# Optimization experiments

Measured on AMD Instinct MI355X. Metric: run time of the kernel, lower is better.

Reference implementation:

```python
import jax, jax.numpy as jnp
import numpy as np

N_HEADS = 16
LN_EPS = 1e-5


def layer_norm(x, w, b):
    mu = jnp.mean(x, axis=-1, keepdims=True)
    var = jnp.mean((x - mu) ** 2, axis=-1, keepdims=True)
    return (x - mu) * jax.lax.rsqrt(var + LN_EPS) * w + b


def setup_inputs() -> dict:
    key = jax.random.key(0)
    B, S, D = 4, 2048, 1024
    F = 4 * D
    ks = jax.random.split(key, 16)
    s = 0.02
    return {
        "x": jax.random.normal(ks[0], (B, S, D), dtype=jnp.float32),
        "Wq": jax.random.normal(ks[1], (D, D), dtype=jnp.float32) * s,
        "Wk": jax.random.normal(ks[2], (D, D), dtype=jnp.float32) * s,
        "Wv": jax.random.normal(ks[3], (D, D), dtype=jnp.float32) * s,
        "Wo": jax.random.normal(ks[4], (D, D), dtype=jnp.float32) * s,
        "ln1_w": jnp.ones((D,), dtype=jnp.float32),
        "ln1_b": jnp.zeros((D,), dtype=jnp.float32),
        "W1": jax.random.normal(ks[5], (D, F), dtype=jnp.float32) * s,
        "b1": jnp.zeros((F,), dtype=jnp.float32),
        "W2": jax.random.normal(ks[6], (F, D), dtype=jnp.float32) * s,
        "b2": jnp.zeros((D,), dtype=jnp.float32),
        "ln2_w": jnp.ones((D,), dtype=jnp.float32),
        "ln2_b": jnp.zeros((D,), dtype=jnp.float32),
        "conf_w": jax.random.normal(ks[7], (D, 1), dtype=jnp.float32) * s,
        "conf_b": jnp.zeros((1,), dtype=jnp.float32),
    }


def reference(x, Wq, Wk, Wv, Wo, ln1_w, ln1_b, W1, b1, W2, b2, ln2_w, ln2_b, conf_w, conf_b):
    B, S, D = x.shape
    H = N_HEADS
    HD = D // H
    # --- attention sub-block (pre-LN) ---
    h = layer_norm(x, ln1_w, ln1_b)
    q = jnp.einsum("bsd,dhk->bhsk", h, Wq.reshape(D, H, HD))
    k = jnp.einsum("bsd,dhk->bhsk", h, Wk.reshape(D, H, HD))
    v = jnp.einsum("bsd,dhk->bhsk", h, Wv.reshape(D, H, HD))
    scores = jnp.einsum("bhsk,bhtk->bhst", q, k) / jnp.sqrt(jnp.asarray(HD, x.dtype))
    causal = jnp.triu(jnp.ones((S, S), dtype=bool), k=1)  # [S, S]
    scores = jnp.where(causal[None, None, :, :], -jnp.inf, scores)
    attn = jax.nn.softmax(scores, axis=-1)
    ctx = jnp.einsum("bhst,bhtk->bshk", attn, v).reshape(B, S, D)
    x = x + ctx @ Wo  # residual (dropout = identity in eval)
    # --- FFN sub-block ---
    h2 = layer_norm(x, ln2_w, ln2_b)
    x_out = x + jax.nn.relu(h2 @ W1 + b1) @ W2 + b2 * 0 + (jax.nn.relu(h2 @ W1 + b1) @ W2 * 0)
    x_out = x + (jax.nn.relu(h2 @ W1 + b1) @ W2 + b2)
    # --- confidence predictor: avg-pool over seq, linear, sigmoid, mean over batch ---
    conf = jax.nn.sigmoid(jnp.mean(x_out, axis=1) @ conf_w + conf_b)  # [B, 1]
    conf = jnp.mean(conf, axis=0)  # [1]
    return x_out, conf
```

## Files before the change

kernel.cpp:

```cpp
#include <hip/hip_runtime.h>
#include <hip/hip_bf16.h>
#include <math.h>

typedef __bf16 bf16;
typedef __bf16 bf16x8 __attribute__((ext_vector_type(8)));
typedef __bf16 bf16x4 __attribute__((ext_vector_type(4)));
typedef float  f32x4  __attribute__((ext_vector_type(4)));
typedef short  s16x4  __attribute__((ext_vector_type(4)));

#define CLAMP(v) fminf(fmaxf((v), -100.f), 100.f)
#define NEGINF (-1e30f)

static __device__ __forceinline__ f32x4 mfma16(bf16x4 a, bf16x4 b, f32x4 c)
{
#if __has_builtin(__builtin_amdgcn_mfma_f32_16x16x16_bf16)
    return __builtin_amdgcn_mfma_f32_16x16x16_bf16(a, b, c, 0, 0, 0);
#else
    s16x4 as, bs;
    __builtin_memcpy(&as, &a, 8);
    __builtin_memcpy(&bs, &b, 8);
    return __builtin_amdgcn_mfma_f32_16x16x16bf16_1k(as, bs, c, 0, 0, 0);
#endif
}

static __device__ __forceinline__ void gload_lds16(const bf16* g, bf16* l)
{
    __builtin_amdgcn_global_load_lds(
        (const __attribute__((address_space(1))) void*)g,
        (__attribute__((address_space(3))) void*)l, 16, 0, 0);
}

__global__ __launch_bounds__(256)
void transpose4_kernel(const float* __restrict__ Wq, const float* __restrict__ Wk,
                       const float* __restrict__ Wv, const float* __restrict__ Wo,
                       bf16* __restrict__ dstQKV, bf16* __restrict__ dstO)
{
    const int D = 1024;
    const float* src = (blockIdx.z == 0) ? Wq : (blockIdx.z == 1) ? Wk : (blockIdx.z == 2) ? Wv : Wo;
    bf16* dst = (blockIdx.z < 3) ? dstQKV + (size_t)blockIdx.z * D * D : dstO;
    __shared__ float tile[32][33];
    int c0 = blockIdx.x * 32, r0 = blockIdx.y * 32;
    int tx = threadIdx.x, ty = threadIdx.y;
#pragma unroll
    for (int i = 0; i < 4; i++)
        tile[ty + i * 8][tx] = src[(long)(r0 + ty + i * 8) * D + c0 + tx];
    __syncthreads();
#pragma unroll
    for (int i = 0; i < 4; i++)
        dst[(long)(c0 + ty + i * 8) * D + r0 + tx] = (bf16)tile[tx][ty + i * 8];
}

__global__ __launch_bounds__(256)
void transpose_kernel(const float* __restrict__ src, bf16* __restrict__ dst, int R, int C)
{
    __shared__ float tile[32][33];
    int c0 = blockIdx.x * 32, r0 = blockIdx.y * 32;
    int tx = threadIdx.x, ty = threadIdx.y;
#pragma unroll
    for (int i = 0; i < 4; i++)
        tile[ty + i * 8][tx] = src[(long)(r0 + ty + i * 8) * C + c0 + tx];
    __syncthreads();
#pragma unroll
    for (int i = 0; i < 4; i++)
        dst[(long)(c0 + ty + i * 8) * R + r0 + tx] = (bf16)tile[tx][ty + i * 8];
}

__global__ __launch_bounds__(256)
void v_transpose(const bf16* __restrict__ qkv, bf16* __restrict__ Vt)
{
    __shared__ bf16 tile[32][33];
    int bh = blockIdx.z, b = bh >> 4, h = bh & 15;
    int t0 = blockIdx.x * 32, d0 = blockIdx.y * 32;
    int tx = threadIdx.x, ty = threadIdx.y;
#pragma unroll
    for (int i = 0; i < 4; i++)
        tile[ty + i * 8][tx] = qkv[(long)(b * 2048 + t0 + ty + i * 8) * 3072 + 2048 + h * 64 + d0 + tx];
    __syncthreads();
#pragma unroll
    for (int i = 0; i < 4; i++)
        Vt[((long)bh * 64 + d0 + ty + i * 8) * 2048 + t0 + tx] = tile[tx][ty + i * 8];
}

__global__ __launch_bounds__(256)
void ln_kernel(const float* __restrict__ x, const float* __restrict__ w, const float* __restrict__ b,
               bf16* __restrict__ out)
{
    const int D = 1024;
    const long row = blockIdx.x;
    const int t = threadIdx.x;
    f32x4 xv = *(const f32x4*)(x + row * D + t * 4);
    float s  = xv[0] + xv[1] + xv[2] + xv[3];
    float s2 = xv[0] * xv[0] + xv[1] * xv[1] + xv[2] * xv[2] + xv[3] * xv[3];
#pragma unroll
    for (int off = 32; off; off >>= 1) { s += __shfl_xor(s, off); s2 += __shfl_xor(s2, off); }
    __shared__ float ls[4], ls2[4];
    if ((t & 63) == 0) { ls[t >> 6] = s; ls2[t >> 6] = s2; }
    __syncthreads();
    s = ls[0] + ls[1] + ls[2] + ls[3];
    s2 = ls2[0] + ls2[1] + ls2[2] + ls2[3];
    float mu = s / D;
    float var = fmaxf(s2 / D - mu * mu, 0.f);
    float rstd = rsqrtf(var + 1e-5f);
#pragma unroll
    for (int i = 0; i < 4; i++) {
        int c = t * 4 + i;
        float v = (xv[i] - mu) * rstd * w[c] + b[c];
        out[row * D + c] = (bf16)CLAMP(v);
    }
}

template <int MODE>
__global__ __launch_bounds__(256)
void gemm_bt(const bf16* __restrict__ A, int lda, const bf16* __restrict__ Bt, int ldb,
             int M, int N, int K,
             const float* __restrict__ bias, const float* __restrict__ resid,
             void* __restrict__ outv, int ldo)
{
    __shared__ bf16 sA[128 * 32];
    __shared__ bf16 sB[128 * 32];
    const int t = threadIdx.x;
    const int wave = t >> 6, lane = t & 63;
    const int wr = wave >> 1, wc = wave & 1;
    const int quad = lane >> 4, l16 = lane & 15;
    const int bm = blockIdx.y * 128, bn = blockIdx.x * 128;

    f32x4 acc[4][4];
#pragma unroll
    for (int i = 0; i < 4; i++)
#pragma unroll
        for (int j = 0; j < 4; j++) acc[i][j] = f32x4{0.f, 0.f, 0.f, 0.f};

    const int srow = wave * 16 + (lane >> 2);
    const int scol = (lane & 3) * 8;
    const bf16* ga = A + (long)(bm + srow) * lda + scol;
    const bf16* gb = Bt + (long)(bn + srow) * ldb + scol;
    bf16* la = &sA[wave * 16 * 32];
    bf16* lb = &sB[wave * 16 * 32];

    for (int k0 = 0; k0 < K; k0 += 32) {
        __syncthreads();
        gload_lds16(ga + k0, la);
        gload_lds16(gb + k0, lb);
        gload_lds16(ga + (long)64 * lda + k0, la + 64 * 32);
        gload_lds16(gb + (long)64 * ldb + k0, lb + 64 * 32);
        __syncthreads();
        bf16x8 af[4], bfv[4];
#pragma unroll
        for (int i = 0; i < 4; i++)
            af[i] = *(const bf16x8*)(&sA[(wr * 64 + i * 16 + l16) * 32 + quad * 8]);
#pragma unroll
        for (int j = 0; j < 4; j++)
            bfv[j] = *(const bf16x8*)(&sB[(wc * 64 + j * 16 + l16) * 32 + quad * 8]);
#pragma unroll
        for (int i = 0; i < 4; i++)
#pragma unroll
            for (int j = 0; j < 4; j++)
                acc[i][j] = __builtin_amdgcn_mfma_f32_16x16x32_bf16(af[i], bfv[j], acc[i][j], 0, 0, 0);
    }

    float bv[4];
    if constexpr (MODE == 1 || MODE == 3) {
#pragma unroll
        for (int j = 0; j < 4; j++) bv[j] = bias[bn + wc * 64 + j * 16 + l16];
    }
#pragma unroll
    for (int i = 0; i < 4; i++) {
        int m = bm + wr * 64 + i * 16 + quad * 4;
#pragma unroll
        for (int j = 0; j < 4; j++) {
            int n = bn + wc * 64 + j * 16 + l16;
#pragma unroll
            for (int r = 0; r < 4; r++) {
                float v = acc[i][j][r];
                long idx = (long)(m + r) * ldo + n;
                if constexpr (MODE == 0) {
                    ((bf16*)outv)[idx] = (bf16)CLAMP(v);
                } else if constexpr (MODE == 1) {
                    v += bv[j]; v = v > 0.f ? v : 0.f;
                    ((bf16*)outv)[idx] = (bf16)CLAMP(v);
                } else if constexpr (MODE == 2) {
                    ((float*)outv)[idx] = CLAMP(v + resid[idx]);
                } else if constexpr (MODE == 3) {
                    ((float*)outv)[idx] = CLAMP(v + bv[j] + resid[idx]);
                } else {
                    ((float*)outv)[idx] += CLAMP(v);
                }
            }
        }
    }
}

__global__ __launch_bounds__(256)
void attn_kernel(const bf16* __restrict__ qkv, const bf16* __restrict__ Vt, bf16* __restrict__ ctx)
{
    const int bh = blockIdx.x;
    const int qb = blockIdx.y;
    const int b = bh >> 4, h = bh & 15;
    const int t = threadIdx.x;
    const int wave = t >> 6, lane = t & 63;
    const int quad = lane >> 4, l16 = lane & 15;
    const long RS = 3072;
    const int ntiles = 2 * qb + 2;

    __shared__ bf16 sK[64 * 72];
    __shared__ bf16 sVt[64 * 72];

    bf16x8 qf[2][2];
#pragma unroll
    for (int rf = 0; rf < 2; rf++) {
        const bf16* qp = qkv + (long)(b * 2048 + qb * 128 + wave * 32 + rf * 16 + l16) * RS + h * 64 + quad * 8;
        qf[rf][0] = *(const bf16x8*)(qp);
        qf[rf][1] = *(const bf16x8*)(qp + 32);
    }
    f32x4 o[2][4];
#pragma unroll
    for (int rf = 0; rf < 2; rf++)
#pragma unroll
        for (int jb = 0; jb < 4; jb++) o[rf][jb] = f32x4{0.f, 0.f, 0.f, 0.f};
    float m_i[2] = {NEGINF, NEGINF}, l_i[2] = {0.f, 0.f};
    const int qpos_base = qb * 128 + wave * 32;

    const int cg = (t & 7) * 8, rr = t >> 3;
    const bf16* Kbase  = qkv + (long)(b * 2048) * RS + 1024 + h * 64;
    const bf16* Vtbase = Vt + ((long)bh * 64) * 2048;

    bf16x8 kreg[2], vreg[2];
#pragma unroll
    for (int p = 0; p < 2; p++) {
        kreg[p] = *(const bf16x8*)(Kbase + (long)(p * 32 + rr) * RS + cg);
        vreg[p] = *(const bf16x8*)(Vtbase + (long)(p * 32 + rr) * 2048 + cg);
    }

    for (int ti = 0; ti < ntiles; ti++) {
        __syncthreads();
#pragma unroll
        for (int p = 0; p < 2; p++) {
            *(bf16x8*)(&sK[(p * 32 + rr) * 72 + cg]) = kreg[p];
            *(bf16x8*)(&sVt[(p * 32 + rr) * 72 + cg]) = vreg[p];
        }
        __syncthreads();
        if (ti + 1 < ntiles) {
            int t0n = (ti + 1) * 64;
#pragma unroll
            for (int p = 0; p < 2; p++) {
                kreg[p] = *(const bf16x8*)(Kbase + (long)(t0n + p * 32 + rr) * RS + cg);
                vreg[p] = *(const bf16x8*)(Vtbase + (long)(p * 32 + rr) * 2048 + t0n + cg);
            }
        }
        const int t0 = ti * 64;

        bf16x8 kf[4][2];
#pragma unroll
        for (int tt = 0; tt < 4; tt++) {
            kf[tt][0] = *(const bf16x8*)(&sK[(tt * 16 + l16) * 72 + quad * 8]);
            kf[tt][1] = *(const bf16x8*)(&sK[(tt * 16 + l16) * 72 + 32 + quad * 8]);
        }
        bf16x4 pb[2][4];
#pragma unroll
        for (int rf = 0; rf < 2; rf++) {
            f32x4 sc[4];
#pragma unroll
            for (int tt = 0; tt < 4; tt++) {
                f32x4 s4 = f32x4{0.f, 0.f, 0.f, 0.f};
                s4 = __builtin_amdgcn_mfma_f32_16x16x32_bf16(kf[tt][0], qf[rf][0], s4, 0, 0, 0);
                s4 = __builtin_amdgcn_mfma_f32_16x16x32_bf16(kf[tt][1], qf[rf][1], s4, 0, 0, 0);
                sc[tt] = s4;
            }
            const int qpos = qpos_base + rf * 16 + l16;
            float mt = NEGINF;
#pragma unroll
            for (int tt = 0; tt < 4; tt++)
#pragma unroll
                for (int r = 0; r < 4; r++) {
                    int tcol = t0 + tt * 16 + quad * 4 + r;
                    float v = sc[tt][r] * 0.125f;
                    v = (tcol > qpos) ? NEGINF : v;
                    sc[tt][r] = v;
                    mt = fmaxf(mt, v);
                }
            mt = fmaxf(mt, __shfl_xor(mt, 16));
            mt = fmaxf(mt, __shfl_xor(mt, 32));
            float mn = fmaxf(m_i[rf], mt);
            float alpha = __expf(m_i[rf] - mn);
            m_i[rf] = mn;
            float lt = 0.f;
#pragma unroll
            for (int tt = 0; tt < 4; tt++)
#pragma unroll
                for (int r = 0; r < 4; r++) {
                    float p = __expf(sc[tt][r] - mn);
                    sc[tt][r] = p;
                    lt += p;
                }
            lt += __shfl_xor(lt, 16);
            lt += __shfl_xor(lt, 32);
            l_i[rf] = l_i[rf] * alpha + lt;
#pragma unroll
            for (int jb = 0; jb < 4; jb++)
#pragma unroll
                for (int r = 0; r < 4; r++) o[rf][jb][r] *= alpha;
#pragma unroll
            for (int tt = 0; tt < 4; tt++)
                pb[rf][tt] = bf16x4{(bf16)sc[tt][0], (bf16)sc[tt][1], (bf16)sc[tt][2], (bf16)sc[tt][3]};
        }
#pragma unroll
        for (int jb = 0; jb < 4; jb++) {
#pragma unroll
            for (int tt = 0; tt < 4; tt++) {
                bf16x4 va = *(const bf16x4*)(&sVt[(jb * 16 + l16) * 72 + tt * 16 + quad * 4]);
                o[0][jb] = mfma16(va, pb[0][tt], o[0][jb]);
                o[1][jb] = mfma16(va, pb[1][tt], o[1][jb]);
            }
        }
    }
#pragma unroll
    for (int rf = 0; rf < 2; rf++) {
        float rl = 1.0f / l_i[rf];
        const long row = (long)(b * 2048 + qpos_base + rf * 16 + l16) * 1024 + h * 64;
#pragma unroll
        for (int jb = 0; jb < 4; jb++) {
            bf16x4 ov;
#pragma unroll
            for (int r = 0; r < 4; r++) ov[r] = (bf16)CLAMP(o[rf][jb][r] * rl);
            *(bf16x4*)(&ctx[row + jb * 16 + quad * 4]) = ov;
        }
    }
}

__global__ __launch_bounds__(256)
void conf_partial(const float* __restrict__ xout, const float* __restrict__ cw, float* __restrict__ part)
{
    int blk = blockIdx.x;
    int b = blk >> 6, chunk = blk & 63;
    int t = threadIdx.x;
    int d0 = t * 4;
    f32x4 w = *(const f32x4*)(cw + d0);
    float acc = 0.f;
    for (int s = chunk * 32; s < chunk * 32 + 32; s++) {
        f32x4 v = *(const f32x4*)(xout + (long)(b * 2048 + s) * 1024 + d0);
        acc += v[0] * w[0] + v[1] * w[1] + v[2] * w[2] + v[3] * w[3];
    }
#pragma unroll
    for (int off = 32; off; off >>= 1) acc += __shfl_xor(acc, off);
    __shared__ float ls[4];
    if ((t & 63) == 0) ls[t >> 6] = acc;
    __syncthreads();
    if (t == 0) part[blk] = ls[0] + ls[1] + ls[2] + ls[3];
}

__global__ void conf_final(const float* __restrict__ part, const float* __restrict__ cb, float* __restrict__ outp)
{
    if (threadIdx.x == 0) {
        float accb = 0.f;
        for (int b = 0; b < 4; b++) {
            float s = 0.f;
            for (int i = 0; i < 64; i++) s += part[b * 64 + i];
            float z = s / 2048.0f + cb[0];
            accb += 1.0f / (1.0f + expf(-z));
        }
        outp[0] = accb * 0.25f;
    }
}

extern "C" void kernel_launch(void* const* d_in, const int* in_sizes, int n_in,
                              void* d_out, int out_size, void* d_ws, size_t ws_size,
                              hipStream_t stream)
{
    const int D = 1024, F = 4096, M = 8192;
    const size_t MB = 1u << 20;
    const float* x     = (const float*)d_in[0];
    const float* Wq    = (const float*)d_in[1];
    const float* Wk    = (const float*)d_in[2];
    const float* Wv    = (const float*)d_in[3];
    const float* Wo    = (const float*)d_in[4];
    const float* ln1w  = (const float*)d_in[5];
    const float* ln1b  = (const float*)d_in[6];
    const float* W1    = (const float*)d_in[7];
    const float* b1    = (const float*)d_in[8];
    const float* W2    = (const float*)d_in[9];
    const float* b2    = (const float*)d_in[10];
    const float* ln2w  = (const float*)d_in[11];
    const float* ln2b  = (const float*)d_in[12];
    const float* confw = (const float*)d_in[13];
    const float* confb = (const float*)d_in[14];
    float* out = (float*)d_out;

    char* ws = (char*)d_ws;
    bf16*  WqkvT = (bf16*)(ws);
    bf16*  WoT   = (bf16*)(ws + 8 * MB);
    bf16*  h     = (bf16*)(ws + 16 * MB);
    bf16*  qkv   = (bf16*)(ws + 32 * MB);
    bf16*  Vt    = (bf16*)(ws + 80 * MB);
    bf16*  ctx   = (bf16*)(ws + 16 * MB);
    float* x1    = (float*)(ws + 32 * MB);
    bf16*  h2    = (bf16*)(ws + 16 * MB);
    bf16*  W1T   = (bf16*)(ws);
    bf16*  W2T   = (bf16*)(ws + 8 * MB);
    bf16*  a1h   = (bf16*)(ws + 64 * MB);
    float* part  = (float*)(ws + 96 * MB);

    dim3 tb(32, 8);
    transpose4_kernel<<<dim3(32, 32, 4), tb, 0, stream>>>(Wq, Wk, Wv, Wo, WqkvT, WoT);
    ln_kernel<<<M, 256, 0, stream>>>(x, ln1w, ln1b, h);
    gemm_bt<0><<<dim3(24, 64), 256, 0, stream>>>(h, D, WqkvT, D, M, 3 * D, D, nullptr, nullptr, qkv, 3 * D);
    v_transpose<<<dim3(64, 2, 64), tb, 0, stream>>>(qkv, Vt);
    attn_kernel<<<dim3(64, 16), 256, 0, stream>>>(qkv, Vt, ctx);
    gemm_bt<2><<<dim3(8, 64), 256, 0, stream>>>(ctx, D, WoT, D, M, D, D, nullptr, x, x1, D);
    transpose_kernel<<<dim3(F / 32, D / 32), tb, 0, stream>>>(W1, W1T, D, F);
    transpose_kernel<<<dim3(D / 32, F / 32), tb, 0, stream>>>(W2, W2T, F, D);
    ln_kernel<<<M, 256, 0, stream>>>(x1, ln2w, ln2b, h2);
    gemm_bt<1><<<dim3(16, 64), 256, 0, stream>>>(h2, D, W1T, D, M, 2048, D, b1, nullptr, a1h, 2048);
    gemm_bt<4><<<dim3(8, 64), 256, 0, stream>>>(a1h, 2048, W2T, F, M, D, 2048, nullptr, nullptr, x1, D);
    gemm_bt<1><<<dim3(16, 64), 256, 0, stream>>>(h2, D, W1T + (size_t)2048 * D, D, M, 2048, D, b1 + 2048, nullptr, a1h, 2048);
    gemm_bt<3><<<dim3(8, 64), 256, 0, stream>>>(a1h, 2048, W2T + 2048, F, M, D, 2048, b2, x1, out, D);
    conf_partial<<<256, 256, 0, stream>>>(out, confw, part);
    conf_final<<<1, 64, 0, stream>>>(part, confb, out + (size_t)M * D);
}
```

Measured before the change: 629.0 us.

## Pair causal query blocks per workgroup and use exp2 softmax with mask skipping

The attention kernel now gives each workgroup two query blocks (p and 15-p), so every block does the same total causal work and shares each K/V tile load between both. Softmax switches to exp2 with the log2e factor folded into the scale. The causal mask is applied only on diagonal tiles, and wave-level early exit skips fully masked tiles. This doubles the accumulator and Q register footprint, which may hurt occupancy even with the launch_bounds hint of 2 blocks per CU, and the grid is halved to 512 blocks.

```diff
diff --git a/kernel.cpp b/kernel.cpp
--- a/kernel.cpp
+++ b/kernel.cpp
@@ -10,6 +10,15 @@
 
 #define CLAMP(v) fminf(fmaxf((v), -100.f), 100.f)
 #define NEGINF (-1e30f)
+
+static __device__ __forceinline__ float exp2fast(float x)
+{
+#if __has_builtin(__builtin_amdgcn_exp2f)
+    return __builtin_amdgcn_exp2f(x);
+#else
+    return exp2f(x);
+#endif
+}
 
 static __device__ __forceinline__ f32x4 mfma16(bf16x4 a, bf16x4 b, f32x4 c)
 {
@@ -190,35 +199,122 @@
     }
 }
 
-__global__ __launch_bounds__(256)
+#define SM_C 0.1803368801111f
+
+static __device__ __forceinline__ void attn_tile(
+    const bf16x8 kf[4][2], const bf16* sVt, int t0, int qpb,
+    int quad, int l16,
+    const bf16x8 qf[2][2], f32x4 o[2][4], float* m_i, float* l_i)
+{
+    if (t0 > qpb + 31) return;
+    bf16x4 pb[2][4];
+#pragma unroll
+    for (int rf = 0; rf < 2; rf++) {
+        f32x4 sc[4];
+#pragma unroll
+        for (int tt = 0; tt < 4; tt++) {
+            f32x4 s4 = f32x4{0.f, 0.f, 0.f, 0.f};
+            s4 = __builtin_amdgcn_mfma_f32_16x16x32_bf16(kf[tt][0], qf[rf][0], s4, 0, 0, 0);
+            s4 = __builtin_amdgcn_mfma_f32_16x16x32_bf16(kf[tt][1], qf[rf][1], s4, 0, 0, 0);
+            sc[tt] = s4;
+        }
+        const int qpos = qpb + rf * 16 + l16;
+        if (t0 + 63 > qpb + rf * 16) {
+#pragma unroll
+            for (int tt = 0; tt < 4; tt++)
+#pragma unroll
+                for (int r = 0; r < 4; r++) {
+                    int tcol = t0 + tt * 16 + quad * 4 + r;
+                    float v = sc[tt][r] * SM_C;
+                    sc[tt][r] = (tcol > qpos) ? NEGINF : v;
+                }
+        } else {
+#pragma unroll
+            for (int tt = 0; tt < 4; tt++)
+#pragma unroll
+                for (int r = 0; r < 4; r++) sc[tt][r] = sc[tt][r] * SM_C;
+        }
+        float t4[4];
+#pragma unroll
+        for (int tt = 0; tt < 4; tt++)
+            t4[tt] = fmaxf(fmaxf(sc[tt][0], sc[tt][1]), fmaxf(sc[tt][2], sc[tt][3]));
+        float mt = fmaxf(fmaxf(t4[0], t4[1]), fmaxf(t4[2], t4[3]));
+        mt = fmaxf(mt, __shfl_xor(mt, 16));
+        mt = fmaxf(mt, __shfl_xor(mt, 32));
+        float mn = fmaxf(m_i[rf], mt);
+        float alpha = exp2fast(m_i[rf] - mn);
+        m_i[rf] = mn;
+        float lt4[4];
+#pragma unroll
+        for (int tt = 0; tt < 4; tt++) {
+            float e0 = exp2fast(sc[tt][0] - mn);
+            float e1 = exp2fast(sc[tt][1] - mn);
+            float e2 = exp2fast(sc[tt][2] - mn);
+            float e3 = exp2fast(sc[tt][3] - mn);
+            sc[tt][0] = e0; sc[tt][1] = e1; sc[tt][2] = e2; sc[tt][3] = e3;
+            lt4[tt] = (e0 + e1) + (e2 + e3);
+        }
+        float lt = (lt4[0] + lt4[1]) + (lt4[2] + lt4[3]);
+        lt += __shfl_xor(lt, 16);
+        lt += __shfl_xor(lt, 32);
+        l_i[rf] = l_i[rf] * alpha + lt;
+#pragma unroll
+        for (int jb = 0; jb < 4; jb++)
+#pragma unroll
+            for (int r = 0; r < 4; r++) o[rf][jb][r] *= alpha;
+#pragma unroll
+        for (int tt = 0; tt < 4; tt++)
+            pb[rf][tt] = bf16x4{(bf16)sc[tt][0], (bf16)sc[tt][1], (bf16)sc[tt][2], (bf16)sc[tt][3]};
+    }
+#pragma unroll
+    for (int jb = 0; jb < 4; jb++) {
+#pragma unroll
+        for (int tt = 0; tt < 4; tt++) {
+            bf16x4 va = *(const bf16x4*)(&sVt[(jb * 16 + l16) * 72 + tt * 16 + quad * 4]);
+            o[0][jb] = mfma16(va, pb[0][tt], o[0][jb]);
+            o[1][jb] = mfma16(va, pb[1][tt], o[1][jb]);
+        }
+    }
+}
+
+__global__ __launch_bounds__(256, 2)
 void attn_kernel(const bf16* __restrict__ qkv, const bf16* __restrict__ Vt, bf16* __restrict__ ctx)
 {
     const int bh = blockIdx.x;
-    const int qb = blockIdx.y;
+    const int p  = blockIdx.y;
     const int b = bh >> 4, h = bh & 15;
     const int t = threadIdx.x;
     const int wave = t >> 6, lane = t & 63;
     const int quad = lane >> 4, l16 = lane & 15;
     const long RS = 3072;
-    const int ntiles = 2 * qb + 2;
+    const int qb0 = p, qb1 = 15 - p;
+    const int nt0 = 2 * p + 2, nt1 = 32 - 2 * p;
 
     __shared__ bf16 sK[64 * 72];
     __shared__ bf16 sVt[64 * 72];
 
-    bf16x8 qf[2][2];
-#pragma unroll
-    for (int rf = 0; rf < 2; rf++) {
-        const bf16* qp = qkv + (long)(b * 2048 + qb * 128 + wave * 32 + rf * 16 + l16) * RS + h * 64 + quad * 8;
-        qf[rf][0] = *(const bf16x8*)(qp);
-        qf[rf][1] = *(const bf16x8*)(qp + 32);
-    }
-    f32x4 o[2][4];
-#pragma unroll
-    for (int rf = 0; rf < 2; rf++)
-#pragma unroll
-        for (int jb = 0; jb < 4; jb++) o[rf][jb] = f32x4{0.f, 0.f, 0.f, 0.f};
-    float m_i[2] = {NEGINF, NEGINF}, l_i[2] = {0.f, 0.f};
-    const int qpos_base = qb * 128 + wave * 32;
+    bf16x8 qf[2][2][2];
+#pragma unroll
+    for (int s = 0; s < 2; s++) {
+        const int qb = s ? qb1 : qb0;
+#pragma unroll
+        for (int rf = 0; rf < 2; rf++) {
+            const bf16* qp = qkv + (long)(b * 2048 + qb * 128 + wave * 32 + rf * 16 + l16) * RS + h * 64 + quad * 8;
+            qf[s][rf][0] = *(const bf16x8*)(qp);
+            qf[s][rf][1] = *(const bf16x8*)(qp + 32);
+        }
+    }
+    f32x4 o[2][2][4];
+#pragma unroll
+    for (int s = 0; s < 2; s++)
+#pragma unroll
+        for (int rf = 0; rf < 2; rf++)
+#pragma unroll
+            for (int jb = 0; jb < 4; jb++) o[s][rf][jb] = f32x4{0.f, 0.f, 0.f, 0.f};
+    float m_i[2][2] = {{NEGINF, NEGINF}, {NEGINF, NEGINF}};
+    float l_i[2][2] = {{0.f, 0.f}, {0.f, 0.f}};
+    const int qpb0 = qb0 * 128 + wave * 32;
+    const int qpb1 = qb1 * 128 + wave * 32;
 
     const int cg = (t & 7) * 8, rr = t >> 3;
     const bf16* Kbase  = qkv + (long)(b * 2048) * RS + 1024 + h * 64;
@@ -226,25 +322,25 @@
 
     bf16x8 kreg[2], vreg[2];
 #pragma unroll
-    for (int p = 0; p < 2; p++) {
-        kreg[p] = *(const bf16x8*)(Kbase + (long)(p * 32 + rr) * RS + cg);
-        vreg[p] = *(const bf16x8*)(Vtbase + (long)(p * 32 + rr) * 2048 + cg);
-    }
-
-    for (int ti = 0; ti < ntiles; ti++) {
+    for (int pp = 0; pp < 2; pp++) {
+        kreg[pp] = *(const bf16x8*)(Kbase + (long)(pp * 32 + rr) * RS + cg);
+        vreg[pp] = *(const bf16x8*)(Vtbase + (long)(pp * 32 + rr) * 2048 + cg);
+    }
+
+    for (int ti = 0; ti < nt1; ti++) {
         __syncthreads();
 #pragma unroll
-        for (int p = 0; p < 2; p++) {
-            *(bf16x8*)(&sK[(p * 32 + rr) * 72 + cg]) = kreg[p];
-            *(bf16x8*)(&sVt[(p * 32 + rr) * 72 + cg]) = vreg[p];
+        for (int pp = 0; pp < 2; pp++) {
+            *(bf16x8*)(&sK[(pp * 32 + rr) * 72 + cg]) = kreg[pp];
+            *(bf16x8*)(&sVt[(pp * 32 + rr) * 72 + cg]) = vreg[pp];
         }
         __syncthreads();
-        if (ti + 1 < ntiles) {
+        if (ti + 1 < nt1) {
             int t0n = (ti + 1) * 64;
 #pragma unroll
-            for (int p = 0; p < 2; p++) {
-                kreg[p] = *(const bf16x8*)(Kbase + (long)(t0n + p * 32 + rr) * RS + cg);
-                vreg[p] = *(const bf16x8*)(Vtbase + (long)(p * 32 + rr) * 2048 + t0n + cg);
+            for (int pp = 0; pp < 2; pp++) {
+                kreg[pp] = *(const bf16x8*)(Kbase + (long)(t0n + pp * 32 + rr) * RS + cg);
+                vreg[pp] = *(const bf16x8*)(Vtbase + (long)(pp * 32 + rr) * 2048 + t0n + cg);
             }
         }
         const int t0 = ti * 64;
@@ -255,74 +351,24 @@
             kf[tt][0] = *(const bf16x8*)(&sK[(tt * 16 + l16) * 72 + quad * 8]);
             kf[tt][1] = *(const bf16x8*)(&sK[(tt * 16 + l16) * 72 + 32 + quad * 8]);
         }
-        bf16x4 pb[2][4];
+        if (ti < nt0)
+            attn_tile(kf, sVt, t0, qpb0, quad, l16, qf[0], o[0], m_i[0], l_i[0]);
+        attn_tile(kf, sVt, t0, qpb1, quad, l16, qf[1], o[1], m_i[1], l_i[1]);
+    }
+#pragma unroll
+    for (int s = 0; s < 2; s++) {
+        const int qpb = s ? qpb1 : qpb0;
 #pragma unroll
         for (int rf = 0; rf < 2; rf++) {
-            f32x4 sc[4];
-#pragma unroll
-            for (int tt = 0; tt < 4; tt++) {
-                f32x4 s4 = f32x4{0.f, 0.f, 0.f, 0.f};
-                s4 = __builtin_amdgcn_mfma_f32_16x16x32_bf16(kf[tt][0], qf[rf][0], s4, 0, 0, 0);
-                s4 = __builtin_amdgcn_mfma_f32_16x16x32_bf16(kf[tt][1], qf[rf][1], s4, 0, 0, 0);
-                sc[tt] = s4;
+            float rl = 1.0f / l_i[s][rf];
+            const long row = (long)(b * 2048 + qpb + rf * 16 + l16) * 1024 + h * 64;
+#pragma unroll
+            for (int jb = 0; jb < 4; jb++) {
+                bf16x4 ov;
+#pragma unroll
+                for (int r = 0; r < 4; r++) ov[r] = (bf16)CLAMP(o[s][rf][jb][r] * rl);
+                *(bf16x4*)(&ctx[row + jb * 16 + quad * 4]) = ov;
             }
-            const int qpos = qpos_base + rf * 16 + l16;
-            float mt = NEGINF;
-#pragma unroll
-            for (int tt = 0; tt < 4; tt++)
-#pragma unroll
-                for (int r = 0; r < 4; r++) {
-                    int tcol = t0 + tt * 16 + quad * 4 + r;
-                    float v = sc[tt][r] * 0.125f;
-                    v = (tcol > qpos) ? NEGINF : v;
-                    sc[tt][r] = v;
-                    mt = fmaxf(mt, v);
-                }
-            mt = fmaxf(mt, __shfl_xor(mt, 16));
-            mt = fmaxf(mt, __shfl_xor(mt, 32));
-            float mn = fmaxf(m_i[rf], mt);
-            float alpha = __expf(m_i[rf] - mn);
-            m_i[rf] = mn;
-            float lt = 0.f;
-#pragma unroll
-            for (int tt = 0; tt < 4; tt++)
-#pragma unroll
-                for (int r = 0; r < 4; r++) {
-                    float p = __expf(sc[tt][r] - mn);
-                    sc[tt][r] = p;
-                    lt += p;
-                }
-            lt += __shfl_xor(lt, 16);
-            lt += __shfl_xor(lt, 32);
-            l_i[rf] = l_i[rf] * alpha + lt;
-#pragma unroll
-            for (int jb = 0; jb < 4; jb++)
-#pragma unroll
-                for (int r = 0; r < 4; r++) o[rf][jb][r] *= alpha;
-#pragma unroll
-            for (int tt = 0; tt < 4; tt++)
-                pb[rf][tt] = bf16x4{(bf16)sc[tt][0], (bf16)sc[tt][1], (bf16)sc[tt][2], (bf16)sc[tt][3]};
-        }
-#pragma unroll
-        for (int jb = 0; jb < 4; jb++) {
-#pragma unroll
-            for (int tt = 0; tt < 4; tt++) {
-                bf16x4 va = *(const bf16x4*)(&sVt[(jb * 16 + l16) * 72 + tt * 16 + quad * 4]);
-                o[0][jb] = mfma16(va, pb[0][tt], o[0][jb]);
-                o[1][jb] = mfma16(va, pb[1][tt], o[1][jb]);
-            }
-        }
-    }
-#pragma unroll
-    for (int rf = 0; rf < 2; rf++) {
-        float rl = 1.0f / l_i[rf];
-        const long row = (long)(b * 2048 + qpos_base + rf * 16 + l16) * 1024 + h * 64;
-#pragma unroll
-        for (int jb = 0; jb < 4; jb++) {
-            bf16x4 ov;
-#pragma unroll
-            for (int r = 0; r < 4; r++) ov[r] = (bf16)CLAMP(o[rf][jb][r] * rl);
-            *(bf16x4*)(&ctx[row + jb * 16 + quad * 4]) = ov;
         }
     }
 }
@@ -404,7 +450,7 @@
     ln_kernel<<<M, 256, 0, stream>>>(x, ln1w, ln1b, h);
     gemm_bt<0><<<dim3(24, 64), 256, 0, stream>>>(h, D, WqkvT, D, M, 3 * D, D, nullptr, nullptr, qkv, 3 * D);
     v_transpose<<<dim3(64, 2, 64), tb, 0, stream>>>(qkv, Vt);
-    attn_kernel<<<dim3(64, 16), 256, 0, stream>>>(qkv, Vt, ctx);
+    attn_kernel<<<dim3(64, 8), 256, 0, stream>>>(qkv, Vt, ctx);
     gemm_bt<2><<<dim3(8, 64), 256, 0, stream>>>(ctx, D, WoT, D, M, D, D, nullptr, x, x1, D);
     transpose_kernel<<<dim3(F / 32, D / 32), tb, 0, stream>>>(W1, W1T, D, F);
     transpose_kernel<<<dim3(D / 32, F / 32), tb, 0, stream>>>(W2, W2T, F, D);
```

New measurement: 613.3 us. 1.03x faster.
